# Kernel tuning notes

Hardware: AMD Instinct MI355X
Metric: run time of the kernel (lower is better)

## Reference

```python
import jax, jax.numpy as jnp
import numpy as np

DIM = 1024
HEADS = 16
HEAD_DIM = DIM // HEADS
SCALE = HEAD_DIM ** -0.5


def setup_inputs() -> dict:
    key = jax.random.key(0)
    ks = jax.random.split(key, 9)
    B, S, D = 2, 2048, DIM
    std = 1.0 / np.sqrt(D)
    Z = jax.random.normal(ks[0], (B, S, D), dtype=jnp.float32)
    Wq = jax.random.uniform(ks[1], (D, D), jnp.float32, -std, std)
    bq = jax.random.uniform(ks[2], (D,), jnp.float32, -std, std)
    Wk = jax.random.uniform(ks[3], (D, D), jnp.float32, -std, std)
    bk = jax.random.uniform(ks[4], (D,), jnp.float32, -std, std)
    Wv = jax.random.uniform(ks[5], (D, D), jnp.float32, -std, std)
    bv = jax.random.uniform(ks[6], (D,), jnp.float32, -std, std)
    Wo = jax.random.uniform(ks[7], (D, D), jnp.float32, -std, std)
    bo = jax.random.uniform(ks[8], (D,), jnp.float32, -std, std)
    return {"Z": Z, "Wq": Wq, "bq": bq, "Wk": Wk, "bk": bk,
            "Wv": Wv, "bv": bv, "Wo": Wo, "bo": bo}


def reference(Z, Wq, bq, Wk, bk, Wv, bv, Wo, bo):
    B, S, D = Z.shape
    H, Hd = HEADS, HEAD_DIM
    # torch Linear: y = x @ W.T + b
    Q = (Z @ Wq.T + bq).reshape(B, S, H, Hd).transpose(0, 2, 1, 3)  # [B,H,S,Hd]
    K = (Z @ Wk.T + bk).reshape(B, S, H, Hd).transpose(0, 2, 1, 3)
    V = (Z @ Wv.T + bv).reshape(B, S, H, Hd).transpose(0, 2, 1, 3)
    scores = jnp.einsum('bhqd,bhkd->bhqk', Q, K) * SCALE  # [B,H,S,S]
    weights = jax.nn.softmax(scores, axis=-1)
    weights = jnp.nan_to_num(weights, nan=0.0)
    # dropout=0.0 -> identity (eval mode)
    out = jnp.einsum('bhqk,bhkd->bhqd', weights, V)  # [B,H,S,Hd]
    out = out.transpose(0, 2, 1, 3).reshape(B, S, D)
    return out @ Wo.T + bo
```

## Files before the change

kernel.cpp:

```cpp
#include <hip/hip_runtime.h>
#include <hip/hip_bf16.h>
#include <stdint.h>

typedef unsigned short u16;
typedef __bf16 bf16x8 __attribute__((ext_vector_type(8)));
typedef float f32x4 __attribute__((ext_vector_type(4)));
typedef float f32x16 __attribute__((ext_vector_type(16)));

#define D_MODEL 1024
#define SEQ     2048
#define NB      2
#define NH      16
#define HD      64
#define M_TOT   (NB*SEQ)
#define QSCALE  (0.125f * 1.44269504088896f)
#define DEFER_THR 8.0f

__device__ __forceinline__ u16 f2bf(float f) {
  union { __bf16 b; u16 u; } cv; cv.b = (__bf16)f; return cv.u;
}
__device__ __forceinline__ float exp2_fast(float x) {
  return __builtin_amdgcn_exp2f(x);
}

__device__ __forceinline__ void async_copy16(void* lds_dst, const void* gsrc) {
  __builtin_amdgcn_global_load_lds(
      (const __attribute__((address_space(1))) unsigned int*)gsrc,
      (__attribute__((address_space(3))) unsigned int*)lds_dst, 16, 0, 0);
}

__device__ __forceinline__ void wait_tile(int kt, int nk) {
  if (kt + 2 < nk)      { asm volatile("s_waitcnt vmcnt(8)" ::: "memory"); }
  else if (kt + 1 < nk) { asm volatile("s_waitcnt vmcnt(4)" ::: "memory"); }
  else                  { asm volatile("s_waitcnt vmcnt(0)" ::: "memory"); }
  __builtin_amdgcn_sched_barrier(0);
  __builtin_amdgcn_s_barrier();
  __builtin_amdgcn_sched_barrier(0);
}

__global__ void cvt_all(const float* __restrict__ Z,  const float* __restrict__ Wq,
                        const float* __restrict__ Wk, const float* __restrict__ Wv,
                        const float* __restrict__ Wo,
                        u16* __restrict__ Zb,  u16* __restrict__ Wqb,
                        u16* __restrict__ Wkb, u16* __restrict__ Wvb,
                        u16* __restrict__ Wob)
{
  int i = blockIdx.x * 256 + threadIdx.x;
  const float* src; u16* dst; int off;
  if (i < (1 << 20)) { src = Z; dst = Zb; off = i; }
  else {
    int j = i - (1 << 20);
    int seg = j >> 18; off = j & ((1 << 18) - 1);
    src = (seg == 0) ? Wq : (seg == 1) ? Wk : (seg == 2) ? Wv : Wo;
    dst = (seg == 0) ? Wqb : (seg == 1) ? Wkb : (seg == 2) ? Wvb : Wob;
  }
  float4 v = reinterpret_cast<const float4*>(src)[off];
  ushort4 o;
  o.x = f2bf(v.x); o.y = f2bf(v.y); o.z = f2bf(v.z); o.w = f2bf(v.w);
  reinterpret_cast<ushort4*>(dst)[off] = o;
}

template<int F32OUT, int TRANSV>
__global__ __launch_bounds__(256, 3)
void gemm_bt(const u16* __restrict__ A,
             const u16* __restrict__ B0, const u16* __restrict__ B1, const u16* __restrict__ B2,
             const float* __restrict__ bias0, const float* __restrict__ bias1, const float* __restrict__ bias2,
             void* __restrict__ C0, void* __restrict__ C1, void* __restrict__ C2,
             float s0, float s1, float s2,
             int M, int N, int K)
{
  (void)M;
  const int z = blockIdx.z;
  const u16* Bt = (z == 0) ? B0 : ((z == 1) ? B1 : B2);
  const float* bias = (z == 0) ? bias0 : ((z == 1) ? bias1 : bias2);
  void* Cout = (z == 0) ? C0 : ((z == 1) ? C1 : C2);
  const float oscl = (z == 0) ? s0 : ((z == 1) ? s1 : s2);
  const bool vswap = TRANSV && (z == 2);

  __shared__ u16 lds_a[3][128*32];
  __shared__ u16 lds_b[3][128*32];

  const int tid = threadIdx.x;
  const int w = tid >> 6, lane = tid & 63;
  const int l15 = lane & 15, lhi = lane >> 4;
  const int m0 = blockIdx.y * 128, n0 = blockIdx.x * 128;
  const int wm = w >> 1, wn = w & 1;

  f32x4 acc[4][4] = {};

  auto stage = [&](int buf, int kt) {
    const int k0 = kt * 32;
    #pragma unroll
    for (int i = 0; i < 2; ++i) {
      const int base = (w*2 + i) * 1024;
      const int pos  = base + (lane << 4);
      const int row  = pos >> 6;
      const int slot = (pos >> 4) & 3;
      const int ss   = slot ^ ((row >> 1) & 3);
      async_copy16((char*)lds_a[buf] + base,
                   (const char*)(A  + (size_t)(m0 + row) * K + k0 + ss*8));
      async_copy16((char*)lds_b[buf] + base,
                   (const char*)(Bt + (size_t)(n0 + row) * K + k0 + ss*8));
    }
  };

  auto compute = [&](int buf) {
    bf16x8 af[4], bf[4];
    #pragma unroll
    for (int mi = 0; mi < 4; ++mi) {
      const int row = wm*64 + mi*16 + l15;
      const int s   = lhi ^ ((row >> 1) & 3);
      af[mi] = *reinterpret_cast<const bf16x8*>((const char*)lds_a[buf] + row*64 + s*16);
    }
    #pragma unroll
    for (int ni = 0; ni < 4; ++ni) {
      const int row = wn*64 + ni*16 + l15;
      const int s   = lhi ^ ((row >> 1) & 3);
      bf[ni] = *reinterpret_cast<const bf16x8*>((const char*)lds_b[buf] + row*64 + s*16);
    }
    if (vswap) {
      #pragma unroll
      for (int mi = 0; mi < 4; ++mi)
        #pragma unroll
        for (int ni = 0; ni < 4; ++ni)
          acc[mi][ni] = __builtin_amdgcn_mfma_f32_16x16x32_bf16(bf[ni], af[mi], acc[mi][ni], 0, 0, 0);
    } else {
      #pragma unroll
      for (int mi = 0; mi < 4; ++mi)
        #pragma unroll
        for (int ni = 0; ni < 4; ++ni)
          acc[mi][ni] = __builtin_amdgcn_mfma_f32_16x16x32_bf16(af[mi], bf[ni], acc[mi][ni], 0, 0, 0);
    }
  };

  const int nk = K >> 5;
  stage(0, 0);
  stage(1, 1);
  for (int kt = 0; kt < nk; ++kt) {
    const int cb = kt % 3;
    if (kt + 2 < nk) stage((kt + 2) % 3, kt + 2);
    wait_tile(kt, nk);
    compute(cb);
    __builtin_amdgcn_sched_barrier(0);
    __builtin_amdgcn_s_barrier();
  }

  if (vswap) {
    #pragma unroll
    for (int mi = 0; mi < 4; ++mi) {
      const int sglob = m0 + wm*64 + mi*16 + l15;
      const int b2 = sglob >> 11, s = sglob & (SEQ - 1);
      #pragma unroll
      for (int ni = 0; ni < 4; ++ni) {
        #pragma unroll
        for (int r = 0; r < 4; ++r) {
          const int dglob = n0 + wn*64 + ni*16 + (lhi << 2) + r;
          const int hh = dglob >> 6, dd = dglob & 63;
          const float v = acc[mi][ni][r] + bias[dglob];
          reinterpret_cast<u16*>(Cout)[((size_t)(b2*NH + hh)*HD + dd)*SEQ + s] = f2bf(v);
        }
      }
    }
  } else {
    #pragma unroll
    for (int mi = 0; mi < 4; ++mi) {
      const int rowb = m0 + wm*64 + mi*16 + (lhi << 2);
      #pragma unroll
      for (int ni = 0; ni < 4; ++ni) {
        const int col = n0 + wn*64 + ni*16 + l15;
        const float bb = bias[col];
        #pragma unroll
        for (int r = 0; r < 4; ++r) {
          const float v = (acc[mi][ni][r] + bb) * oscl;
          if (F32OUT)
            reinterpret_cast<float*>(Cout)[(size_t)(rowb + r) * N + col] = v;
          else
            reinterpret_cast<u16*>(Cout)[(size_t)(rowb + r) * N + col] = f2bf(v);
        }
      }
    }
  }
}

__global__ __launch_bounds__(256, 2)
void attn32(const u16* __restrict__ Qb, const u16* __restrict__ Kb,
            const u16* __restrict__ Vt, u16* __restrict__ Ob)
{
  __shared__ u16 vt[3][64*64];
  __shared__ u16 kt[3][64*64];

  const int tid = threadIdx.x;
  const int w = tid >> 6, lane = tid & 63;
  const int l31 = lane & 31, hi = lane >> 5;
  const int bh = blockIdx.y, b = bh >> 4, h = bh & 15;
  const int qrow = blockIdx.x * 128 + w * 32 + l31;

  bf16x8 qf[4];
  {
    const u16* qp = Qb + (size_t)(b*SEQ + qrow) * D_MODEL + h*HD + hi*8;
    #pragma unroll
    for (int kc = 0; kc < 4; ++kc)
      qf[kc] = *reinterpret_cast<const bf16x8*>(qp + kc*16);
  }

  const u16* Vtg = Vt + (size_t)bh * HD * SEQ;
  const u16* Kg  = Kb + (size_t)(b*SEQ) * D_MODEL + h*HD;

  float mrun = -1e30f, lrun = 0.f;
  f32x16 o0 = {}, o1 = {};

  auto stageKV = [&](int buf, int kv0) {
    #pragma unroll
    for (int i = 0; i < 2; ++i) {
      const int c = i*256 + tid;
      const int d = c >> 3;
      const int sl = c & 7;
      const int sg = sl ^ (d & 7);
      async_copy16((char*)vt[buf] + (size_t)(i*256 + w*64)*16,
                   (const char*)(Vtg + (size_t)d*SEQ + kv0 + sg*8));
    }
    #pragma unroll
    for (int i = 0; i < 2; ++i) {
      const int c = i*256 + tid;
      const int key = c >> 3;
      const int sl = c & 7;
      const int sg = sl ^ (key & 7);
      async_copy16((char*)kt[buf] + (size_t)(i*256 + w*64)*16,
                   (const char*)(Kg + (size_t)(kv0 + key)*D_MODEL + sg*8));
    }
  };

  const int nt = SEQ / 64;
  stageKV(0, 0);
  stageKV(1, 64);

  for (int t = 0; t < nt; ++t) {
    const int cb = t % 3;
    if (t + 2 < nt) stageKV((t + 2) % 3, (t + 2) * 64);
    wait_tile(t, nt);

    f32x16 s0 = {}, s1 = {};
    {
      const char* kbp = (const char*)kt[cb];
      #pragma unroll
      for (int kc = 0; kc < 4; ++kc) {
        const int sw = (kc*2 + hi) ^ (l31 & 7);
        bf16x8 ka0 = *reinterpret_cast<const bf16x8*>(kbp + (size_t)(l31*8 + sw)*16);
        s0 = __builtin_amdgcn_mfma_f32_32x32x16_bf16(ka0, qf[kc], s0, 0, 0, 0);
        bf16x8 ka1 = *reinterpret_cast<const bf16x8*>(kbp + (size_t)((l31+32)*8 + sw)*16);
        s1 = __builtin_amdgcn_mfma_f32_32x32x16_bf16(ka1, qf[kc], s1, 0, 0, 0);
      }
    }

    float tmax = s0[0];
    #pragma unroll
    for (int r = 1; r < 16; ++r) tmax = fmaxf(tmax, s0[r]);
    #pragma unroll
    for (int r = 0; r < 16; ++r) tmax = fmaxf(tmax, s1[r]);
    tmax = fmaxf(tmax, __shfl_xor(tmax, 32));
    if (!__all(tmax - mrun <= DEFER_THR)) {
      const float mnew = fmaxf(mrun, tmax);
      const float a = exp2_fast(mrun - mnew);
      lrun *= a;
      #pragma unroll
      for (int r = 0; r < 16; ++r) { o0[r] *= a; o1[r] *= a; }
      mrun = mnew;
    }
    float rs = 0.f;
    #pragma unroll
    for (int r = 0; r < 16; ++r) { s0[r] = exp2_fast(s0[r] - mrun); rs += s0[r]; }
    #pragma unroll
    for (int r = 0; r < 16; ++r) { s1[r] = exp2_fast(s1[r] - mrun); rs += s1[r]; }
    rs += __shfl_xor(rs, 32);
    lrun += rs;

    unsigned pwA[2][8];
    #pragma unroll
    for (int a4 = 0; a4 < 4; ++a4)
      #pragma unroll
      for (int zz = 0; zz < 2; ++zz) {
        pwA[0][a4*2+zz] = (unsigned)f2bf(s0[4*a4+2*zz]) | ((unsigned)f2bf(s0[4*a4+2*zz+1]) << 16);
        pwA[1][a4*2+zz] = (unsigned)f2bf(s1[4*a4+2*zz]) | ((unsigned)f2bf(s1[4*a4+2*zz+1]) << 16);
      }

    const char* vb = (const char*)vt[cb];
    #pragma unroll
    for (int ks = 0; ks < 4; ++ks) {
      const int kb = ks >> 1, sm = ks & 1;
      unsigned keep0 = hi ? pwA[kb][(2*sm+1)*2+0] : pwA[kb][(2*sm)*2+0];
      unsigned keep1 = hi ? pwA[kb][(2*sm+1)*2+1] : pwA[kb][(2*sm)*2+1];
      unsigned send0 = hi ? pwA[kb][(2*sm)*2+0]   : pwA[kb][(2*sm+1)*2+0];
      unsigned send1 = hi ? pwA[kb][(2*sm)*2+1]   : pwA[kb][(2*sm+1)*2+1];
      unsigned recv0 = (unsigned)__shfl_xor((int)send0, 32);
      unsigned recv1 = (unsigned)__shfl_xor((int)send1, 32);
      union { bf16x8 f; unsigned u[4]; } pf;
      pf.u[0] = hi ? recv0 : keep0;
      pf.u[1] = hi ? recv1 : keep1;
      pf.u[2] = hi ? keep0 : recv0;
      pf.u[3] = hi ? keep1 : recv1;

      const int slg = ks*2 + hi;
      const int sw  = slg ^ (l31 & 7);
      bf16x8 va0 = *reinterpret_cast<const bf16x8*>(vb + (size_t)(l31*8 + sw)*16);
      bf16x8 va1 = *reinterpret_cast<const bf16x8*>(vb + (size_t)((l31+32)*8 + sw)*16);

      o0 = __builtin_amdgcn_mfma_f32_32x32x16_bf16(va0, pf.f, o0, 0, 0, 0);
      o1 = __builtin_amdgcn_mfma_f32_32x32x16_bf16(va1, pf.f, o1, 0, 0, 0);
    }

    __builtin_amdgcn_sched_barrier(0);
    __builtin_amdgcn_s_barrier();
  }

  const float inv = 1.0f / lrun;
  u16* op = Ob + (size_t)(b*SEQ + qrow) * D_MODEL + h*HD;
  #pragma unroll
  for (int a4 = 0; a4 < 4; ++a4) {
    ushort4 v0, v1;
    v0.x = f2bf(o0[4*a4+0]*inv); v0.y = f2bf(o0[4*a4+1]*inv);
    v0.z = f2bf(o0[4*a4+2]*inv); v0.w = f2bf(o0[4*a4+3]*inv);
    v1.x = f2bf(o1[4*a4+0]*inv); v1.y = f2bf(o1[4*a4+1]*inv);
    v1.z = f2bf(o1[4*a4+2]*inv); v1.w = f2bf(o1[4*a4+3]*inv);
    *reinterpret_cast<ushort4*>(op + 8*a4 + 4*hi)      = v0;
    *reinterpret_cast<ushort4*>(op + 32 + 8*a4 + 4*hi) = v1;
  }
}

extern "C" void kernel_launch(void* const* d_in, const int* in_sizes, int n_in,
                              void* d_out, int out_size, void* d_ws, size_t ws_size,
                              hipStream_t stream)
{
  (void)in_sizes; (void)n_in; (void)out_size;
  const float* Z  = (const float*)d_in[0];
  const float* Wq = (const float*)d_in[1];
  const float* bq = (const float*)d_in[2];
  const float* Wk = (const float*)d_in[3];
  const float* bk = (const float*)d_in[4];
  const float* Wv = (const float*)d_in[5];
  const float* bv = (const float*)d_in[6];
  const float* Wo = (const float*)d_in[7];
  const float* bo = (const float*)d_in[8];
  float* out = (float*)d_out;

  const size_t needed = (size_t)(M_TOT*D_MODEL)*2*5 + (size_t)(D_MODEL*D_MODEL)*2*4;
  if (ws_size < needed) return;

  u16* Zb  = (u16*)d_ws;
  u16* Wqb = Zb  + (size_t)M_TOT*D_MODEL;
  u16* Wkb = Wqb + (size_t)D_MODEL*D_MODEL;
  u16* Wvb = Wkb + (size_t)D_MODEL*D_MODEL;
  u16* Wob = Wvb + (size_t)D_MODEL*D_MODEL;
  u16* Qb  = Wob + (size_t)D_MODEL*D_MODEL;
  u16* Kb  = Qb  + (size_t)M_TOT*D_MODEL;
  u16* Vt  = Kb  + (size_t)M_TOT*D_MODEL;
  u16* Ab  = Vt  + (size_t)M_TOT*D_MODEL;

  cvt_all<<<dim3(8192), 256, 0, stream>>>(Z, Wq, Wk, Wv, Wo, Zb, Wqb, Wkb, Wvb, Wob);

  dim3 gproj(D_MODEL/128, M_TOT/128, 3);
  gemm_bt<0,1><<<gproj, 256, 0, stream>>>(Zb, Wqb, Wkb, Wvb, bq, bk, bv,
                                          (void*)Qb, (void*)Kb, (void*)Vt,
                                          QSCALE, 1.0f, 1.0f,
                                          M_TOT, D_MODEL, D_MODEL);

  dim3 gattn(SEQ/128, NB*NH);
  attn32<<<gattn, 256, 0, stream>>>(Qb, Kb, Vt, Ab);

  dim3 gout(D_MODEL/128, M_TOT/128, 1);
  gemm_bt<1,0><<<gout, 256, 0, stream>>>(Ab, Wob, Wob, Wob, bo, bo, bo,
                                         (void*)out, (void*)out, (void*)out,
                                         1.0f, 1.0f, 1.0f,
                                         M_TOT, D_MODEL, D_MODEL);
}
```

Before: 237.2 us.

## Retile projection and output GEMMs to 256x256 blocks with 512 threads

Replaces the 128x128, BK=32, triple-buffered GEMM with a 256x256-tile, BK=64, double-buffered kernel using 512 threads, 128KB of dynamic LDS and an 8-slot XOR swizzle. Global and LDS offsets are now precomputed once outside the K loop. The aim is more data reuse per LDS load and fewer loop iterations. The cost is a much smaller grid (192 blocks for QKV, 64 for the output projection), which cannot fill all CUs. The 128KB LDS also limits occupancy to one block per CU.

```diff
diff --git a/kernel.cpp b/kernel.cpp
--- a/kernel.cpp
+++ b/kernel.cpp
@@ -27,15 +27,6 @@
   __builtin_amdgcn_global_load_lds(
       (const __attribute__((address_space(1))) unsigned int*)gsrc,
       (__attribute__((address_space(3))) unsigned int*)lds_dst, 16, 0, 0);
-}
-
-__device__ __forceinline__ void wait_tile(int kt, int nk) {
-  if (kt + 2 < nk)      { asm volatile("s_waitcnt vmcnt(8)" ::: "memory"); }
-  else if (kt + 1 < nk) { asm volatile("s_waitcnt vmcnt(4)" ::: "memory"); }
-  else                  { asm volatile("s_waitcnt vmcnt(0)" ::: "memory"); }
-  __builtin_amdgcn_sched_barrier(0);
-  __builtin_amdgcn_s_barrier();
-  __builtin_amdgcn_sched_barrier(0);
 }
 
 __global__ void cvt_all(const float* __restrict__ Z,  const float* __restrict__ Wq,
@@ -61,12 +52,12 @@
 }
 
 template<int F32OUT, int TRANSV>
-__global__ __launch_bounds__(256, 3)
-void gemm_bt(const u16* __restrict__ A,
+__global__ __launch_bounds__(512, 2)
+void gemm256(const u16* __restrict__ A,
              const u16* __restrict__ B0, const u16* __restrict__ B1, const u16* __restrict__ B2,
              const float* __restrict__ bias0, const float* __restrict__ bias1, const float* __restrict__ bias2,
              void* __restrict__ C0, void* __restrict__ C1, void* __restrict__ C2,
-             float s0, float s1, float s2,
+             float s0f, float s1f, float s2f,
              int M, int N, int K)
 {
   (void)M;
@@ -74,81 +65,97 @@
   const u16* Bt = (z == 0) ? B0 : ((z == 1) ? B1 : B2);
   const float* bias = (z == 0) ? bias0 : ((z == 1) ? bias1 : bias2);
   void* Cout = (z == 0) ? C0 : ((z == 1) ? C1 : C2);
-  const float oscl = (z == 0) ? s0 : ((z == 1) ? s1 : s2);
+  const float oscl = (z == 0) ? s0f : ((z == 1) ? s1f : s2f);
   const bool vswap = TRANSV && (z == 2);
 
-  __shared__ u16 lds_a[3][128*32];
-  __shared__ u16 lds_b[3][128*32];
+  extern __shared__ u16 smem[];
+  char* La = (char*)smem;
+  char* Lb = (char*)smem + 65536;
 
   const int tid = threadIdx.x;
   const int w = tid >> 6, lane = tid & 63;
   const int l15 = lane & 15, lhi = lane >> 4;
-  const int m0 = blockIdx.y * 128, n0 = blockIdx.x * 128;
-  const int wm = w >> 1, wn = w & 1;
-
-  f32x4 acc[4][4] = {};
+  const int m0 = blockIdx.y * 256, n0 = blockIdx.x * 256;
+  const int wm = w >> 2, wn = w & 3;
+
+  f32x4 acc[8][4] = {};
+
+  int aoff[4], boff[4];
+  #pragma unroll
+  for (int i = 0; i < 4; ++i) {
+    const int c = i*512 + tid;
+    const int row = c >> 3;
+    const int sl  = c & 7;
+    const int sg  = sl ^ (row & 7);
+    aoff[i] = (m0 + row) * K + sg*8;
+    boff[i] = (n0 + row) * K + sg*8;
+  }
+  const int ldsoff0 = (0*512 + w*64)*16, ldsoff1 = (1*512 + w*64)*16,
+            ldsoff2 = (2*512 + w*64)*16, ldsoff3 = (3*512 + w*64)*16;
 
   auto stage = [&](int buf, int kt) {
-    const int k0 = kt * 32;
-    #pragma unroll
-    for (int i = 0; i < 2; ++i) {
-      const int base = (w*2 + i) * 1024;
-      const int pos  = base + (lane << 4);
-      const int row  = pos >> 6;
-      const int slot = (pos >> 4) & 3;
-      const int ss   = slot ^ ((row >> 1) & 3);
-      async_copy16((char*)lds_a[buf] + base,
-                   (const char*)(A  + (size_t)(m0 + row) * K + k0 + ss*8));
-      async_copy16((char*)lds_b[buf] + base,
-                   (const char*)(Bt + (size_t)(n0 + row) * K + k0 + ss*8));
-    }
+    const int ko = kt << 6;
+    const int bb = buf * 32768;
+    async_copy16(La + bb + ldsoff0, A  + (size_t)(aoff[0] + ko));
+    async_copy16(Lb + bb + ldsoff0, Bt + (size_t)(boff[0] + ko));
+    async_copy16(La + bb + ldsoff1, A  + (size_t)(aoff[1] + ko));
+    async_copy16(Lb + bb + ldsoff1, Bt + (size_t)(boff[1] + ko));
+    async_copy16(La + bb + ldsoff2, A  + (size_t)(aoff[2] + ko));
+    async_copy16(Lb + bb + ldsoff2, Bt + (size_t)(boff[2] + ko));
+    async_copy16(La + bb + ldsoff3, A  + (size_t)(aoff[3] + ko));
+    async_copy16(Lb + bb + ldsoff3, Bt + (size_t)(boff[3] + ko));
   };
 
+  const int s0 = lhi ^ (l15 & 7);
+  const int abase = (wm*128 + l15)*128 + s0*16;
+  const int bbase = (wn*64  + l15)*128 + s0*16;
+
   auto compute = [&](int buf) {
-    bf16x8 af[4], bf[4];
-    #pragma unroll
-    for (int mi = 0; mi < 4; ++mi) {
-      const int row = wm*64 + mi*16 + l15;
-      const int s   = lhi ^ ((row >> 1) & 3);
-      af[mi] = *reinterpret_cast<const bf16x8*>((const char*)lds_a[buf] + row*64 + s*16);
-    }
-    #pragma unroll
-    for (int ni = 0; ni < 4; ++ni) {
-      const int row = wn*64 + ni*16 + l15;
-      const int s   = lhi ^ ((row >> 1) & 3);
-      bf[ni] = *reinterpret_cast<const bf16x8*>((const char*)lds_b[buf] + row*64 + s*16);
-    }
-    if (vswap) {
-      #pragma unroll
-      for (int mi = 0; mi < 4; ++mi)
-        #pragma unroll
-        for (int ni = 0; ni < 4; ++ni)
-          acc[mi][ni] = __builtin_amdgcn_mfma_f32_16x16x32_bf16(bf[ni], af[mi], acc[mi][ni], 0, 0, 0);
-    } else {
-      #pragma unroll
-      for (int mi = 0; mi < 4; ++mi)
-        #pragma unroll
-        for (int ni = 0; ni < 4; ++ni)
-          acc[mi][ni] = __builtin_amdgcn_mfma_f32_16x16x32_bf16(af[mi], bf[ni], acc[mi][ni], 0, 0, 0);
+    const int bb = buf * 32768;
+    #pragma unroll
+    for (int ks = 0; ks < 2; ++ks) {
+      const int pa = bb + (abase ^ (ks << 6));
+      const int pb = bb + (bbase ^ (ks << 6));
+      bf16x8 bf[4];
+      #pragma unroll
+      for (int ni = 0; ni < 4; ++ni)
+        bf[ni] = *reinterpret_cast<const bf16x8*>(Lb + pb + ni*2048);
+      #pragma unroll
+      for (int mi = 0; mi < 8; ++mi) {
+        bf16x8 af = *reinterpret_cast<const bf16x8*>(La + pa + mi*2048);
+        if (vswap) {
+          #pragma unroll
+          for (int ni = 0; ni < 4; ++ni)
+            acc[mi][ni] = __builtin_amdgcn_mfma_f32_16x16x32_bf16(bf[ni], af, acc[mi][ni], 0, 0, 0);
+        } else {
+          #pragma unroll
+          for (int ni = 0; ni < 4; ++ni)
+            acc[mi][ni] = __builtin_amdgcn_mfma_f32_16x16x32_bf16(af, bf[ni], acc[mi][ni], 0, 0, 0);
+        }
+      }
     }
   };
 
-  const int nk = K >> 5;
+  const int nt = K >> 6;
   stage(0, 0);
   stage(1, 1);
-  for (int kt = 0; kt < nk; ++kt) {
-    const int cb = kt % 3;
-    if (kt + 2 < nk) stage((kt + 2) % 3, kt + 2);
-    wait_tile(kt, nk);
+  for (int t = 0; t < nt; ++t) {
+    const int cb = t & 1;
+    if (t + 1 < nt) { asm volatile("s_waitcnt vmcnt(8)" ::: "memory"); }
+    else            { asm volatile("s_waitcnt vmcnt(0)" ::: "memory"); }
+    __builtin_amdgcn_sched_barrier(0);
+    __builtin_amdgcn_s_barrier();
+    __builtin_amdgcn_sched_barrier(0);
     compute(cb);
     __builtin_amdgcn_sched_barrier(0);
     __builtin_amdgcn_s_barrier();
+    if (t + 2 < nt) stage(cb, t + 2);
   }
 
   if (vswap) {
     #pragma unroll
-    for (int mi = 0; mi < 4; ++mi) {
-      const int sglob = m0 + wm*64 + mi*16 + l15;
+    for (int mi = 0; mi < 8; ++mi) {
+      const int sglob = m0 + wm*128 + mi*16 + l15;
       const int b2 = sglob >> 11, s = sglob & (SEQ - 1);
       #pragma unroll
       for (int ni = 0; ni < 4; ++ni) {
@@ -163,8 +170,8 @@
     }
   } else {
     #pragma unroll
-    for (int mi = 0; mi < 4; ++mi) {
-      const int rowb = m0 + wm*64 + mi*16 + (lhi << 2);
+    for (int mi = 0; mi < 8; ++mi) {
+      const int rowb = m0 + wm*128 + mi*16 + (lhi << 2);
       #pragma unroll
       for (int ni = 0; ni < 4; ++ni) {
         const int col = n0 + wn*64 + ni*16 + l15;
@@ -237,7 +244,12 @@
   for (int t = 0; t < nt; ++t) {
     const int cb = t % 3;
     if (t + 2 < nt) stageKV((t + 2) % 3, (t + 2) * 64);
-    wait_tile(t, nt);
+    if (t + 2 < nt)      { asm volatile("s_waitcnt vmcnt(8)" ::: "memory"); }
+    else if (t + 1 < nt) { asm volatile("s_waitcnt vmcnt(4)" ::: "memory"); }
+    else                 { asm volatile("s_waitcnt vmcnt(0)" ::: "memory"); }
+    __builtin_amdgcn_sched_barrier(0);
+    __builtin_amdgcn_s_barrier();
+    __builtin_amdgcn_sched_barrier(0);
 
     f32x16 s0 = {}, s1 = {};
     {
@@ -357,18 +369,20 @@
 
   cvt_all<<<dim3(8192), 256, 0, stream>>>(Z, Wq, Wk, Wv, Wo, Zb, Wqb, Wkb, Wvb, Wob);
 
-  dim3 gproj(D_MODEL/128, M_TOT/128, 3);
-  gemm_bt<0,1><<<gproj, 256, 0, stream>>>(Zb, Wqb, Wkb, Wvb, bq, bk, bv,
-                                          (void*)Qb, (void*)Kb, (void*)Vt,
-                                          QSCALE, 1.0f, 1.0f,
-                                          M_TOT, D_MODEL, D_MODEL);
+  const size_t lds_bytes = 131072;
+
+  dim3 gproj(D_MODEL/256, M_TOT/256, 3);
+  gemm256<0,1><<<gproj, 512, lds_bytes, stream>>>(Zb, Wqb, Wkb, Wvb, bq, bk, bv,
+                                                  (void*)Qb, (void*)Kb, (void*)Vt,
+                                                  QSCALE, 1.0f, 1.0f,
+                                                  M_TOT, D_MODEL, D_MODEL);
 
   dim3 gattn(SEQ/128, NB*NH);
   attn32<<<gattn, 256, 0, stream>>>(Qb, Kb, Vt, Ab);
 
-  dim3 gout(D_MODEL/128, M_TOT/128, 1);
-  gemm_bt<1,0><<<gout, 256, 0, stream>>>(Ab, Wob, Wob, Wob, bo, bo, bo,
-                                         (void*)out, (void*)out, (void*)out,
-                                         1.0f, 1.0f, 1.0f,
-                                         M_TOT, D_MODEL, D_MODEL);
-}
+  dim3 gout(D_MODEL/256, M_TOT/256, 1);
+  gemm256<1,0><<<gout, 512, lds_bytes, stream>>>(Ab, Wob, Wob, Wob, bo, bo, bo,
+                                                 (void*)out, (void*)out, (void*)out,
+                                                 1.0f, 1.0f, 1.0f,
+                                                 M_TOT, D_MODEL, D_MODEL);
+}
```

Result: slower. 247.3 us (+4.2%).
